# Kernel optimization log

Hardware: AMD Instinct MI355X
Metric: run time of the kernel (lower is better)

## Reference

```python
import jax, jax.numpy as jnp
import numpy as np

B, S, E, FFN, Q = 8, 2048, 512, 2048, 8


def setup_inputs() -> dict:
    key = jax.random.key(0)
    k0, k1, k2, k3 = jax.random.split(key, 4)
    x = jax.random.normal(k0, (B, S, E), dtype=jnp.float32)
    ry = jax.random.normal(k1, (Q,), dtype=jnp.float32)  # trainable RY angles
    w1 = jax.random.normal(k2, (FFN, Q), dtype=jnp.float32) / np.sqrt(Q).astype(np.float32)
    b1 = jnp.zeros((FFN,), dtype=jnp.float32)
    w2 = jax.random.normal(k3, (E, FFN), dtype=jnp.float32) / np.sqrt(FFN).astype(np.float32)
    b2 = jnp.zeros((E,), dtype=jnp.float32)
    return {"x": x, "ry": ry, "w1": w1, "b1": b1, "w2": w2, "b2": b2}


def reference(x, ry, w1, b1, w2, b2):
    # Quantum layer: each qubit i starts in |0>, gets RX(x[..., i]) then RY(ry[i]),
    # then PauliZ expectation. Product state => closed form <Z_i> = cos(x_i) * cos(ry_i).
    nq = ry.shape[0]
    z = jnp.cos(x[..., :nq]) * jnp.cos(ry)  # [B, S, Q]
    # dropout is identity in eval mode
    h = jnp.einsum("bsq,fq->bsf", z, w1) + b1  # fc1
    return jnp.einsum("bsf,ef->bse", jax.nn.relu(h), w2) + b2  # fc2
```

## Files before the change

### kernel.cpp

```cpp
#include <hip/hip_runtime.h>
#include <cstdint>
#include <cstddef>


typedef __attribute__((ext_vector_type(8))) short s16x8;
typedef __attribute__((ext_vector_type(4))) float f32x4;

__device__ __forceinline__ unsigned short f2bf(float f) {
  unsigned int u = __float_as_uint(f);
  unsigned int r = u + 0x7fffu + ((u >> 16) & 1u);
  return (unsigned short)(r >> 16);
}

__device__ __forceinline__ void async_copy16(const void* g, void* l) {
  __builtin_amdgcn_global_load_lds(
      (const __attribute__((address_space(1))) void*)(uintptr_t)g,
      (__attribute__((address_space(3))) void*)(unsigned int)(uintptr_t)l,
      16, 0, 0);
}

__global__ __launch_bounds__(256) void k_w2(const float* __restrict__ w2,
                                            unsigned short* __restrict__ img) {
  const int n = blockIdx.x;
  const int t = threadIdx.x;
  const int s = t >> 2, quad = t & 3;
  const float* src = w2 + (size_t)n * 2048 + t * 8;
  float4 a = *(const float4*)src;
  float4 b = *(const float4*)(src + 4);
  uint4 pk;
  pk.x = f2bf(a.x) | ((unsigned)f2bf(a.y) << 16);
  pk.y = f2bf(a.z) | ((unsigned)f2bf(a.w) << 16);
  pk.z = f2bf(b.x) | ((unsigned)f2bf(b.y) << 16);
  pk.w = f2bf(b.z) | ((unsigned)f2bf(b.w) << 16);
  const int nt = n >> 8, nl = n & 255, nhi = nl >> 4, nlo = nl & 15;
  const size_t ci = (size_t)(nt * 64 + s) * 1024 + nhi * 64 + quad * 16 + nlo;
  *(uint4*)(img + ci * 8) = pk;
}

__global__ __launch_bounds__(256, 2) void k_fused(
    const float* __restrict__ x, const float* __restrict__ ry,
    const float* __restrict__ w1, const float* __restrict__ b1,
    const unsigned short* __restrict__ w2b, const float* __restrict__ b2,
    float* __restrict__ C) {
  __shared__ unsigned short As[2][64 * 32];
  __shared__ unsigned short Bs[3][256 * 32];
  __shared__ float b1s[2048];

  const int t = threadIdx.x;
  const int lane = t & 63;
  const int w = t >> 6;
  const int mt = (int)(blockIdx.x >> 1);
  const int nt = (int)(blockIdx.x & 1);
  const int r0 = mt * 64;
  const int c0 = nt * 256;
  const int fp = t & 15;
  const int rq = t >> 4;

  float zr[4][8];
  {
    float4 ra = *(const float4*)ry;
    float4 rb = *(const float4*)(ry + 4);
    float cy[8] = {__cosf(ra.x), __cosf(ra.y), __cosf(ra.z), __cosf(ra.w),
                   __cosf(rb.x), __cosf(rb.y), __cosf(rb.z), __cosf(rb.w)};
#pragma unroll
    for (int r = 0; r < 4; ++r) {
      const float* xr = x + (size_t)(r0 + rq * 4 + r) * 512;
      float4 x0 = *(const float4*)xr;
      float4 x1 = *(const float4*)(xr + 4);
      zr[r][0] = __cosf(x0.x) * cy[0];
      zr[r][1] = __cosf(x0.y) * cy[1];
      zr[r][2] = __cosf(x0.z) * cy[2];
      zr[r][3] = __cosf(x0.w) * cy[3];
      zr[r][4] = __cosf(x1.x) * cy[4];
      zr[r][5] = __cosf(x1.y) * cy[5];
      zr[r][6] = __cosf(x1.z) * cy[6];
      zr[r][7] = __cosf(x1.w) * cy[7];
    }
  }
  __builtin_amdgcn_sched_barrier(0);

  const unsigned short* gB = w2b + (size_t)nt * 524288 + t * 8;
  char* lB = (char*)Bs + t * 16;
  auto stage = [&](int s, int buf) {
#pragma unroll
    for (int p = 0; p < 4; ++p)
      async_copy16(gB + (size_t)s * 8192 + p * 2048,
                   lB + buf * 16384 + p * 4096);
  };
  async_copy16(b1 + (size_t)t * 4, (char*)b1s + (size_t)t * 16);
  async_copy16(b1 + (size_t)(t + 256) * 4, (char*)b1s + (size_t)(t + 256) * 16);
  stage(0, 0);
  stage(1, 1);
  __builtin_amdgcn_sched_barrier(0);

  f32x4 wA0, wA1, wA2, wA3, wB0, wB1, wB2, wB3;
  {
    const f32x4* p0 = (const f32x4*)(w1 + fp * 16);
    wA0 = p0[0]; wA1 = p0[1]; wA2 = p0[2]; wA3 = p0[3];
    const f32x4* p1 = (const f32x4*)(w1 + 256 + fp * 16);
    wB0 = p1[0]; wB1 = p1[1]; wB2 = p1[2]; wB3 = p1[3];
  }

  asm volatile("s_waitcnt vmcnt(12) lgkmcnt(0)" ::: "memory");
  __builtin_amdgcn_sched_barrier(0);
  __builtin_amdgcn_s_barrier();

  const int q0 = rq & 1;
  const int koct = fp >> 2, fpl = fp & 3;
  const int sA_off = ((koct ^ ((rq * 2) & 3)) << 4) + fpl * 4;
  const int sB_off = ((koct ^ ((rq * 2 + 1) & 3)) << 4) + fpl * 4;
  const int rw0 = ((rq * 4 + 0) ^ q0) * 64;
  const int rw1 = ((rq * 4 + 1) ^ q0) * 64;
  const int rw2 = ((rq * 4 + 2) ^ q0) * 64;
  const int rw3 = ((rq * 4 + 3) ^ q0) * 64;

  auto act = [&](int s, int buf, const f32x4& v0, const f32x4& v1,
                 const f32x4& v2, const f32x4& v3) {
    const float bb0 = b1s[s * 32 + fp * 2];
    const float bb1 = b1s[s * 32 + fp * 2 + 1];
    unsigned int u0, u1, u2, u3;
#define ACT_ROW(R, UD)                                                      \
  {                                                                         \
    float h0 = bb0, h1 = bb1;                                               \
    h0 += zr[R][0] * v0[0]; h1 += zr[R][0] * v2[0];                         \
    h0 += zr[R][1] * v0[1]; h1 += zr[R][1] * v2[1];                         \
    h0 += zr[R][2] * v0[2]; h1 += zr[R][2] * v2[2];                         \
    h0 += zr[R][3] * v0[3]; h1 += zr[R][3] * v2[3];                         \
    h0 += zr[R][4] * v1[0]; h1 += zr[R][4] * v3[0];                         \
    h0 += zr[R][5] * v1[1]; h1 += zr[R][5] * v3[1];                         \
    h0 += zr[R][6] * v1[2]; h1 += zr[R][6] * v3[2];                         \
    h0 += zr[R][7] * v1[3]; h1 += zr[R][7] * v3[3];                         \
    h0 = fmaxf(h0, 0.0f);                                                   \
    h1 = fmaxf(h1, 0.0f);                                                   \
    asm("v_cvt_pk_bf16_f32 %0, %1, %2" : "=v"(UD) : "v"(h0), "v"(h1));      \
  }
    ACT_ROW(0, u0) ACT_ROW(1, u1) ACT_ROW(2, u2) ACT_ROW(3, u3)
#undef ACT_ROW
    char* base = (char*)As + buf * 4096;
    *(unsigned int*)(base + rw0 + sA_off) = q0 ? u1 : u0;
    *(unsigned int*)(base + rw1 + sA_off) = q0 ? u0 : u1;
    *(unsigned int*)(base + rw2 + sB_off) = q0 ? u3 : u2;
    *(unsigned int*)(base + rw3 + sB_off) = q0 ? u2 : u3;
  };

  act(0, 0, wA0, wA1, wA2, wA3);

  const int wn = w * 64;
  const int fr = lane & 15;
  const int quad = lane >> 4;
  const char* pAb =
      (const char*)As + fr * 64 + ((quad ^ ((fr >> 1) & 3)) << 4);
  const char* pBb = (const char*)Bs + w * 4096 + quad * 256 + fr * 16;

  f32x4 acc[4][4];
#pragma unroll
  for (int i = 0; i < 4; ++i)
#pragma unroll
    for (int j = 0; j < 4; ++j) acc[i][j] = (f32x4){0.f, 0.f, 0.f, 0.f};

#define BODY(KT, BUF, BUF2, L0, L1, L2, L3, U0, U1, U2, U3, PRE, ACTG, VMC) \
  {                                                                         \
    asm volatile("s_waitcnt vmcnt(" VMC ") lgkmcnt(0)" ::: "memory");       \
    __builtin_amdgcn_sched_barrier(0);                                      \
    __builtin_amdgcn_s_barrier();                                           \
    if (PRE) {                                                              \
      stage((KT) + 2, BUF2);                                                \
      const f32x4* wp =                                                     \
          (const f32x4*)(w1 + (size_t)((KT) + 2) * 256 + fp * 16);          \
      L0 = wp[0]; L1 = wp[1]; L2 = wp[2]; L3 = wp[3];                       \
    }                                                                       \
    s16x8 af[4], bfv[4];                                                    \
    {                                                                       \
      const char* pA = pAb + ((KT) & 1) * 4096;                             \
      const char* pB = pBb + (BUF) * 16384;                                 \
      af[0] = *(const s16x8*)(pA);                                          \
      af[1] = *(const s16x8*)(pA + 1024);                                   \
      af[2] = *(const s16x8*)(pA + 2048);                                   \
      af[3] = *(const s16x8*)(pA + 3072);                                   \
      bfv[0] = *(const s16x8*)(pB);                                         \
      bfv[1] = *(const s16x8*)(pB + 1024);                                  \
      bfv[2] = *(const s16x8*)(pB + 2048);                                  \
      bfv[3] = *(const s16x8*)(pB + 3072);                                  \
    }                                                                       \
    if (ACTG) act((KT) + 1, ((KT) + 1) & 1, U0, U1, U2, U3);                \
    __builtin_amdgcn_s_setprio(1);                                          \
    _Pragma("unroll") for (int i = 0; i < 4; ++i)                           \
        _Pragma("unroll") for (int j = 0; j < 4; ++j) acc[i][j] =           \
        __builtin_amdgcn_mfma_f32_16x16x32_bf16(af[i], bfv[j], acc[i][j],   \
                                                0, 0, 0);                   \
    __builtin_amdgcn_s_setprio(0);                                          \
  }

  for (int kt = 0; kt < 60; kt += 6) {
    BODY(kt + 0, 0, 2, wA0, wA1, wA2, wA3, wB0, wB1, wB2, wB3, true, true, "8");
    BODY(kt + 1, 1, 0, wB0, wB1, wB2, wB3, wA0, wA1, wA2, wA3, true, true, "8");
    BODY(kt + 2, 2, 1, wA0, wA1, wA2, wA3, wB0, wB1, wB2, wB3, true, true, "8");
    BODY(kt + 3, 0, 2, wB0, wB1, wB2, wB3, wA0, wA1, wA2, wA3, true, true, "8");
    BODY(kt + 4, 1, 0, wA0, wA1, wA2, wA3, wB0, wB1, wB2, wB3, true, true, "8");
    BODY(kt + 5, 2, 1, wB0, wB1, wB2, wB3, wA0, wA1, wA2, wA3, true, true, "8");
  }
  BODY(60, 0, 2, wA0, wA1, wA2, wA3, wB0, wB1, wB2, wB3, true, true, "8");
  BODY(61, 1, 0, wB0, wB1, wB2, wB3, wA0, wA1, wA2, wA3, true, true, "8");
  BODY(62, 2, 1, wA0, wA1, wA2, wA3, wB0, wB1, wB2, wB3, false, true, "8");
  BODY(63, 0, 2, wB0, wB1, wB2, wB3, wA0, wA1, wA2, wA3, false, false, "4");
#undef BODY

  float bias[4];
#pragma unroll
  for (int j = 0; j < 4; ++j) bias[j] = b2[c0 + wn + j * 16 + fr];
#pragma unroll
  for (int i = 0; i < 4; ++i) {
    const int rbase = r0 + i * 16 + quad * 4;
#pragma unroll
    for (int rr = 0; rr < 4; ++rr) {
      float* crow = C + (size_t)(rbase + rr) * 512;
#pragma unroll
      for (int j = 0; j < 4; ++j)
        crow[c0 + wn + j * 16 + fr] = acc[i][j][rr] + bias[j];
    }
  }
}

__global__ __launch_bounds__(256) void k_naive(
    const float* __restrict__ x, const float* __restrict__ ry,
    const float* __restrict__ w1, const float* __restrict__ b1,
    const float* __restrict__ w2, const float* __restrict__ b2,
    float* __restrict__ out) {
  __shared__ float zsh[8];
  __shared__ float acts[2048];
  const int r = blockIdx.x;
  const int t = threadIdx.x;
  if (t < 8) zsh[t] = __cosf(x[(size_t)r * 512 + t]) * __cosf(ry[t]);
  __syncthreads();
  float z[8];
#pragma unroll
  for (int q = 0; q < 8; ++q) z[q] = zsh[q];
#pragma unroll
  for (int i = 0; i < 8; ++i) {
    const int f = t * 8 + i;
    const float* wr = w1 + (size_t)f * 8;
    float4 a = *(const float4*)wr;
    float4 b = *(const float4*)(wr + 4);
    float h = b1[f] + z[0] * a.x + z[1] * a.y + z[2] * a.z + z[3] * a.w +
              z[4] * b.x + z[5] * b.y + z[6] * b.z + z[7] * b.w;
    acts[f] = fmaxf(h, 0.0f);
  }
  __syncthreads();
  for (int ee = 0; ee < 2; ++ee) {
    const int e = t + ee * 256;
    const float* wr = w2 + (size_t)e * 2048;
    float acc = b2[e];
    for (int f = 0; f < 2048; f += 4) {
      float4 wv = *(const float4*)(wr + f);
      float4 av = *(const float4*)(acts + f);
      acc += av.x * wv.x + av.y * wv.y + av.z * wv.z + av.w * wv.w;
    }
    out[(size_t)r * 512 + e] = acc;
  }
}

extern "C" void kernel_launch(void* const* d_in, const int* in_sizes, int n_in,
                              void* d_out, int out_size, void* d_ws,
                              size_t ws_size, hipStream_t stream) {
  const float* x  = (const float*)d_in[0];
  const float* ry = (const float*)d_in[1];
  const float* w1 = (const float*)d_in[2];
  const float* b1 = (const float*)d_in[3];
  const float* w2 = (const float*)d_in[4];
  const float* b2 = (const float*)d_in[5];
  float* out = (float*)d_out;

  const size_t w2b_bytes = (size_t)512 * 2048 * 2;
  if (ws_size < w2b_bytes) {
    k_naive<<<dim3(16384), dim3(256), 0, stream>>>(x, ry, w1, b1, w2, b2, out);
    return;
  }
  unsigned short* w2b = (unsigned short*)d_ws;
  k_w2<<<dim3(512), dim3(256), 0, stream>>>(w2, w2b);
  k_fused<<<dim3(512), dim3(256), 0, stream>>>(x, ry, w1, b1, w2b, b2, out);
}
```

Measured before the change: 150.7 us.

## Double block to 512 threads, splitting M across two warp groups

Raises the fused kernel to 512 threads per block, with 8 waves arranged 2 (M) by 4 (N). Each thread now computes two activation rows instead of four and holds half the accumulators, and each thread issues half as many async copies per stage. The waitcnt thresholds and the LDS swizzle for A are reworked to match. The aim is more waves per CU to hide latency and lower per-thread register pressure, at the cost of more barrier participants and a __launch_bounds__(512,4) occupancy target that may force register spills.

```diff
diff --git a/kernel.cpp b/kernel.cpp
--- a/kernel.cpp
+++ b/kernel.cpp
@@ -37,7 +37,7 @@
   *(uint4*)(img + ci * 8) = pk;
 }
 
-__global__ __launch_bounds__(256, 2) void k_fused(
+__global__ __launch_bounds__(512, 4) void k_fused(
     const float* __restrict__ x, const float* __restrict__ ry,
     const float* __restrict__ w1, const float* __restrict__ b1,
     const unsigned short* __restrict__ w2b, const float* __restrict__ b2,
@@ -54,17 +54,17 @@
   const int r0 = mt * 64;
   const int c0 = nt * 256;
   const int fp = t & 15;
-  const int rq = t >> 4;
-
-  float zr[4][8];
+  const int rw = t >> 4;
+
+  float zr[2][8];
   {
     float4 ra = *(const float4*)ry;
     float4 rb = *(const float4*)(ry + 4);
     float cy[8] = {__cosf(ra.x), __cosf(ra.y), __cosf(ra.z), __cosf(ra.w),
                    __cosf(rb.x), __cosf(rb.y), __cosf(rb.z), __cosf(rb.w)};
 #pragma unroll
-    for (int r = 0; r < 4; ++r) {
-      const float* xr = x + (size_t)(r0 + rq * 4 + r) * 512;
+    for (int r = 0; r < 2; ++r) {
+      const float* xr = x + (size_t)(r0 + rw * 2 + r) * 512;
       float4 x0 = *(const float4*)xr;
       float4 x1 = *(const float4*)(xr + 4);
       zr[r][0] = __cosf(x0.x) * cy[0];
@@ -82,43 +82,35 @@
   const unsigned short* gB = w2b + (size_t)nt * 524288 + t * 8;
   char* lB = (char*)Bs + t * 16;
   auto stage = [&](int s, int buf) {
-#pragma unroll
-    for (int p = 0; p < 4; ++p)
-      async_copy16(gB + (size_t)s * 8192 + p * 2048,
-                   lB + buf * 16384 + p * 4096);
+    async_copy16(gB + (size_t)s * 8192, lB + buf * 16384);
+    async_copy16(gB + (size_t)s * 8192 + 4096, lB + buf * 16384 + 8192);
   };
   async_copy16(b1 + (size_t)t * 4, (char*)b1s + (size_t)t * 16);
-  async_copy16(b1 + (size_t)(t + 256) * 4, (char*)b1s + (size_t)(t + 256) * 16);
   stage(0, 0);
-  stage(1, 1);
-  __builtin_amdgcn_sched_barrier(0);
-
   f32x4 wA0, wA1, wA2, wA3, wB0, wB1, wB2, wB3;
   {
     const f32x4* p0 = (const f32x4*)(w1 + fp * 16);
     wA0 = p0[0]; wA1 = p0[1]; wA2 = p0[2]; wA3 = p0[3];
+  }
+  stage(1, 1);
+  {
     const f32x4* p1 = (const f32x4*)(w1 + 256 + fp * 16);
     wB0 = p1[0]; wB1 = p1[1]; wB2 = p1[2]; wB3 = p1[3];
   }
 
-  asm volatile("s_waitcnt vmcnt(12) lgkmcnt(0)" ::: "memory");
+  asm volatile("s_waitcnt vmcnt(6) lgkmcnt(0)" ::: "memory");
   __builtin_amdgcn_sched_barrier(0);
   __builtin_amdgcn_s_barrier();
 
-  const int q0 = rq & 1;
   const int koct = fp >> 2, fpl = fp & 3;
-  const int sA_off = ((koct ^ ((rq * 2) & 3)) << 4) + fpl * 4;
-  const int sB_off = ((koct ^ ((rq * 2 + 1) & 3)) << 4) + fpl * 4;
-  const int rw0 = ((rq * 4 + 0) ^ q0) * 64;
-  const int rw1 = ((rq * 4 + 1) ^ q0) * 64;
-  const int rw2 = ((rq * 4 + 2) ^ q0) * 64;
-  const int rw3 = ((rq * 4 + 3) ^ q0) * 64;
+  const int s_off = ((koct ^ (rw & 3)) << 4) + fpl * 4;
+  char* aswr = (char*)As + rw * 128 + s_off;
 
   auto act = [&](int s, int buf, const f32x4& v0, const f32x4& v1,
                  const f32x4& v2, const f32x4& v3) {
     const float bb0 = b1s[s * 32 + fp * 2];
     const float bb1 = b1s[s * 32 + fp * 2 + 1];
-    unsigned int u0, u1, u2, u3;
+    unsigned int u0, u1;
 #define ACT_ROW(R, UD)                                                      \
   {                                                                         \
     float h0 = bb0, h1 = bb1;                                               \
@@ -134,27 +126,26 @@
     h1 = fmaxf(h1, 0.0f);                                                   \
     asm("v_cvt_pk_bf16_f32 %0, %1, %2" : "=v"(UD) : "v"(h0), "v"(h1));      \
   }
-    ACT_ROW(0, u0) ACT_ROW(1, u1) ACT_ROW(2, u2) ACT_ROW(3, u3)
+    ACT_ROW(0, u0) ACT_ROW(1, u1)
 #undef ACT_ROW
-    char* base = (char*)As + buf * 4096;
-    *(unsigned int*)(base + rw0 + sA_off) = q0 ? u1 : u0;
-    *(unsigned int*)(base + rw1 + sA_off) = q0 ? u0 : u1;
-    *(unsigned int*)(base + rw2 + sB_off) = q0 ? u3 : u2;
-    *(unsigned int*)(base + rw3 + sB_off) = q0 ? u2 : u3;
+    char* dst = aswr + buf * 4096;
+    *(unsigned int*)(dst) = u0;
+    *(unsigned int*)(dst + 64) = u1;
   };
 
   act(0, 0, wA0, wA1, wA2, wA3);
 
-  const int wn = w * 64;
+  const int wm = (w >> 2) * 32;
+  const int wn = (w & 3) * 64;
   const int fr = lane & 15;
   const int quad = lane >> 4;
-  const char* pAb =
-      (const char*)As + fr * 64 + ((quad ^ ((fr >> 1) & 3)) << 4);
-  const char* pBb = (const char*)Bs + w * 4096 + quad * 256 + fr * 16;
-
-  f32x4 acc[4][4];
-#pragma unroll
-  for (int i = 0; i < 4; ++i)
+  const char* pAb = (const char*)As + wm * 64 + fr * 64 +
+                    ((quad ^ ((fr >> 1) & 3)) << 4);
+  const char* pBb = (const char*)Bs + (w & 3) * 4096 + quad * 256 + fr * 16;
+
+  f32x4 acc[2][4];
+#pragma unroll
+  for (int i = 0; i < 2; ++i)
 #pragma unroll
     for (int j = 0; j < 4; ++j) acc[i][j] = (f32x4){0.f, 0.f, 0.f, 0.f};
 
@@ -169,14 +160,12 @@
           (const f32x4*)(w1 + (size_t)((KT) + 2) * 256 + fp * 16);          \
       L0 = wp[0]; L1 = wp[1]; L2 = wp[2]; L3 = wp[3];                       \
     }                                                                       \
-    s16x8 af[4], bfv[4];                                                    \
+    s16x8 af[2], bfv[4];                                                    \
     {                                                                       \
       const char* pA = pAb + ((KT) & 1) * 4096;                             \
       const char* pB = pBb + (BUF) * 16384;                                 \
       af[0] = *(const s16x8*)(pA);                                          \
       af[1] = *(const s16x8*)(pA + 1024);                                   \
-      af[2] = *(const s16x8*)(pA + 2048);                                   \
-      af[3] = *(const s16x8*)(pA + 3072);                                   \
       bfv[0] = *(const s16x8*)(pB);                                         \
       bfv[1] = *(const s16x8*)(pB + 1024);                                  \
       bfv[2] = *(const s16x8*)(pB + 2048);                                  \
@@ -184,7 +173,7 @@
     }                                                                       \
     if (ACTG) act((KT) + 1, ((KT) + 1) & 1, U0, U1, U2, U3);                \
     __builtin_amdgcn_s_setprio(1);                                          \
-    _Pragma("unroll") for (int i = 0; i < 4; ++i)                           \
+    _Pragma("unroll") for (int i = 0; i < 2; ++i)                           \
         _Pragma("unroll") for (int j = 0; j < 4; ++j) acc[i][j] =           \
         __builtin_amdgcn_mfma_f32_16x16x32_bf16(af[i], bfv[j], acc[i][j],   \
                                                 0, 0, 0);                   \
@@ -192,25 +181,25 @@
   }
 
   for (int kt = 0; kt < 60; kt += 6) {
-    BODY(kt + 0, 0, 2, wA0, wA1, wA2, wA3, wB0, wB1, wB2, wB3, true, true, "8");
-    BODY(kt + 1, 1, 0, wB0, wB1, wB2, wB3, wA0, wA1, wA2, wA3, true, true, "8");
-    BODY(kt + 2, 2, 1, wA0, wA1, wA2, wA3, wB0, wB1, wB2, wB3, true, true, "8");
-    BODY(kt + 3, 0, 2, wB0, wB1, wB2, wB3, wA0, wA1, wA2, wA3, true, true, "8");
-    BODY(kt + 4, 1, 0, wA0, wA1, wA2, wA3, wB0, wB1, wB2, wB3, true, true, "8");
-    BODY(kt + 5, 2, 1, wB0, wB1, wB2, wB3, wA0, wA1, wA2, wA3, true, true, "8");
-  }
-  BODY(60, 0, 2, wA0, wA1, wA2, wA3, wB0, wB1, wB2, wB3, true, true, "8");
-  BODY(61, 1, 0, wB0, wB1, wB2, wB3, wA0, wA1, wA2, wA3, true, true, "8");
-  BODY(62, 2, 1, wA0, wA1, wA2, wA3, wB0, wB1, wB2, wB3, false, true, "8");
-  BODY(63, 0, 2, wB0, wB1, wB2, wB3, wA0, wA1, wA2, wA3, false, false, "4");
+    BODY(kt + 0, 0, 2, wA0, wA1, wA2, wA3, wB0, wB1, wB2, wB3, true, true, "6");
+    BODY(kt + 1, 1, 0, wB0, wB1, wB2, wB3, wA0, wA1, wA2, wA3, true, true, "6");
+    BODY(kt + 2, 2, 1, wA0, wA1, wA2, wA3, wB0, wB1, wB2, wB3, true, true, "6");
+    BODY(kt + 3, 0, 2, wB0, wB1, wB2, wB3, wA0, wA1, wA2, wA3, true, true, "6");
+    BODY(kt + 4, 1, 0, wA0, wA1, wA2, wA3, wB0, wB1, wB2, wB3, true, true, "6");
+    BODY(kt + 5, 2, 1, wB0, wB1, wB2, wB3, wA0, wA1, wA2, wA3, true, true, "6");
+  }
+  BODY(60, 0, 2, wA0, wA1, wA2, wA3, wB0, wB1, wB2, wB3, true, true, "6");
+  BODY(61, 1, 0, wB0, wB1, wB2, wB3, wA0, wA1, wA2, wA3, true, true, "6");
+  BODY(62, 2, 1, wA0, wA1, wA2, wA3, wB0, wB1, wB2, wB3, false, true, "6");
+  BODY(63, 0, 2, wB0, wB1, wB2, wB3, wA0, wA1, wA2, wA3, false, false, "0");
 #undef BODY
 
   float bias[4];
 #pragma unroll
   for (int j = 0; j < 4; ++j) bias[j] = b2[c0 + wn + j * 16 + fr];
 #pragma unroll
-  for (int i = 0; i < 4; ++i) {
-    const int rbase = r0 + i * 16 + quad * 4;
+  for (int i = 0; i < 2; ++i) {
+    const int rbase = r0 + wm + i * 16 + quad * 4;
 #pragma unroll
     for (int rr = 0; rr < 4; ++rr) {
       float* crow = C + (size_t)(rbase + rr) * 512;
@@ -277,5 +266,5 @@
   }
   unsigned short* w2b = (unsigned short*)d_ws;
   k_w2<<<dim3(512), dim3(256), 0, stream>>>(w2, w2b);
-  k_fused<<<dim3(512), dim3(256), 0, stream>>>(x, ry, w1, b1, w2b, b2, out);
-}
+  k_fused<<<dim3(512), dim3(512), 0, stream>>>(x, ry, w1, b1, w2b, b2, out);
+}
```

After: 177.8 us. +18.0%, slower.

## Load W2 fragments directly from global into registers instead of LDS staging

Applied to the files above, without the earlier changes.

Drops the triple-buffered LDS staging of the pre-packed bf16 W2 tiles. Each wave now loads its MFMA B fragments straight from global memory into registers, double-buffered one k-step ahead. The barrier schedule changes to match: wait on vmcnt before the MFMAs and put a single barrier at the end of each step. This removes LDS traffic and frees LDS for occupancy, at the cost of exposing global-load latency with only one step of prefetch and using more registers.

```diff
diff --git a/kernel.cpp b/kernel.cpp
--- a/kernel.cpp
+++ b/kernel.cpp
@@ -43,7 +43,6 @@
     const unsigned short* __restrict__ w2b, const float* __restrict__ b2,
     float* __restrict__ C) {
   __shared__ unsigned short As[2][64 * 32];
-  __shared__ unsigned short Bs[3][256 * 32];
   __shared__ float b1s[2048];
 
   const int t = threadIdx.x;
@@ -55,6 +54,8 @@
   const int c0 = nt * 256;
   const int fp = t & 15;
   const int rq = t >> 4;
+  const int fr = lane & 15;
+  const int quad = lane >> 4;
 
   float zr[4][8];
   {
@@ -79,20 +80,22 @@
   }
   __builtin_amdgcn_sched_barrier(0);
 
-  const unsigned short* gB = w2b + (size_t)nt * 524288 + t * 8;
-  char* lB = (char*)Bs + t * 16;
-  auto stage = [&](int s, int buf) {
-#pragma unroll
-    for (int p = 0; p < 4; ++p)
-      async_copy16(gB + (size_t)s * 8192 + p * 2048,
-                   lB + buf * 16384 + p * 4096);
-  };
+  const char* gBb =
+      (const char*)w2b +
+      ((size_t)nt * 64 * 1024 + (size_t)w * 256 + quad * 16 + fr) * 16;
+#define LOADB(S, D)                                        \
+  {                                                        \
+    const char* p_ = gBb + (size_t)(S) * 16384;            \
+    D[0] = *(const s16x8*)(p_);                            \
+    D[1] = *(const s16x8*)(p_ + 1024);                     \
+    D[2] = *(const s16x8*)(p_ + 2048);                     \
+    D[3] = *(const s16x8*)(p_ + 3072);                     \
+  }
+
   async_copy16(b1 + (size_t)t * 4, (char*)b1s + (size_t)t * 16);
   async_copy16(b1 + (size_t)(t + 256) * 4, (char*)b1s + (size_t)(t + 256) * 16);
-  stage(0, 0);
-  stage(1, 1);
-  __builtin_amdgcn_sched_barrier(0);
-
+  s16x8 Bp[4], Bq[4];
+  LOADB(0, Bp);
   f32x4 wA0, wA1, wA2, wA3, wB0, wB1, wB2, wB3;
   {
     const f32x4* p0 = (const f32x4*)(w1 + fp * 16);
@@ -100,8 +103,7 @@
     const f32x4* p1 = (const f32x4*)(w1 + 256 + fp * 16);
     wB0 = p1[0]; wB1 = p1[1]; wB2 = p1[2]; wB3 = p1[3];
   }
-
-  asm volatile("s_waitcnt vmcnt(12) lgkmcnt(0)" ::: "memory");
+  asm volatile("s_waitcnt vmcnt(0) lgkmcnt(0)" ::: "memory");
   __builtin_amdgcn_sched_barrier(0);
   __builtin_amdgcn_s_barrier();
 
@@ -144,13 +146,13 @@
   };
 
   act(0, 0, wA0, wA1, wA2, wA3);
+  asm volatile("s_waitcnt lgkmcnt(0)" ::: "memory");
+  __builtin_amdgcn_sched_barrier(0);
+  __builtin_amdgcn_s_barrier();
 
   const int wn = w * 64;
-  const int fr = lane & 15;
-  const int quad = lane >> 4;
   const char* pAb =
       (const char*)As + fr * 64 + ((quad ^ ((fr >> 1) & 3)) << 4);
-  const char* pBb = (const char*)Bs + w * 4096 + quad * 256 + fr * 16;
 
   f32x4 acc[4][4];
 #pragma unroll
@@ -158,52 +160,49 @@
 #pragma unroll
     for (int j = 0; j < 4; ++j) acc[i][j] = (f32x4){0.f, 0.f, 0.f, 0.f};
 
-#define BODY(KT, BUF, BUF2, L0, L1, L2, L3, U0, U1, U2, U3, PRE, ACTG, VMC) \
+#define BODY(KT, BU, BL, WU0, WU1, WU2, WU3, WL0, WL1, WL2, WL3, BPRE,      \
+             WPRE, ACTG, VMC)                                               \
   {                                                                         \
-    asm volatile("s_waitcnt vmcnt(" VMC ") lgkmcnt(0)" ::: "memory");       \
-    __builtin_amdgcn_sched_barrier(0);                                      \
-    __builtin_amdgcn_s_barrier();                                           \
-    if (PRE) {                                                              \
-      stage((KT) + 2, BUF2);                                                \
+    if (BPRE) LOADB((KT) + 1, BL);                                          \
+    if (WPRE) {                                                             \
       const f32x4* wp =                                                     \
           (const f32x4*)(w1 + (size_t)((KT) + 2) * 256 + fp * 16);          \
-      L0 = wp[0]; L1 = wp[1]; L2 = wp[2]; L3 = wp[3];                       \
+      WL0 = wp[0]; WL1 = wp[1]; WL2 = wp[2]; WL3 = wp[3];                   \
     }                                                                       \
-    s16x8 af[4], bfv[4];                                                    \
+    asm volatile("s_waitcnt vmcnt(" VMC ")" ::: "memory");                  \
+    __builtin_amdgcn_sched_barrier(0);                                      \
+    s16x8 af[4];                                                            \
     {                                                                       \
       const char* pA = pAb + ((KT) & 1) * 4096;                             \
-      const char* pB = pBb + (BUF) * 16384;                                 \
       af[0] = *(const s16x8*)(pA);                                          \
       af[1] = *(const s16x8*)(pA + 1024);                                   \
       af[2] = *(const s16x8*)(pA + 2048);                                   \
       af[3] = *(const s16x8*)(pA + 3072);                                   \
-      bfv[0] = *(const s16x8*)(pB);                                         \
-      bfv[1] = *(const s16x8*)(pB + 1024);                                  \
-      bfv[2] = *(const s16x8*)(pB + 2048);                                  \
-      bfv[3] = *(const s16x8*)(pB + 3072);                                  \
     }                                                                       \
-    if (ACTG) act((KT) + 1, ((KT) + 1) & 1, U0, U1, U2, U3);                \
+    if (ACTG) act((KT) + 1, ((KT) + 1) & 1, WU0, WU1, WU2, WU3);            \
+    asm volatile("s_waitcnt lgkmcnt(0)" ::: "memory");                      \
+    __builtin_amdgcn_sched_barrier(0);                                      \
     __builtin_amdgcn_s_setprio(1);                                          \
     _Pragma("unroll") for (int i = 0; i < 4; ++i)                           \
         _Pragma("unroll") for (int j = 0; j < 4; ++j) acc[i][j] =           \
-        __builtin_amdgcn_mfma_f32_16x16x32_bf16(af[i], bfv[j], acc[i][j],   \
+        __builtin_amdgcn_mfma_f32_16x16x32_bf16(af[i], BU[j], acc[i][j],    \
                                                 0, 0, 0);                   \
     __builtin_amdgcn_s_setprio(0);                                          \
-  }
-
-  for (int kt = 0; kt < 60; kt += 6) {
-    BODY(kt + 0, 0, 2, wA0, wA1, wA2, wA3, wB0, wB1, wB2, wB3, true, true, "8");
-    BODY(kt + 1, 1, 0, wB0, wB1, wB2, wB3, wA0, wA1, wA2, wA3, true, true, "8");
-    BODY(kt + 2, 2, 1, wA0, wA1, wA2, wA3, wB0, wB1, wB2, wB3, true, true, "8");
-    BODY(kt + 3, 0, 2, wB0, wB1, wB2, wB3, wA0, wA1, wA2, wA3, true, true, "8");
-    BODY(kt + 4, 1, 0, wA0, wA1, wA2, wA3, wB0, wB1, wB2, wB3, true, true, "8");
-    BODY(kt + 5, 2, 1, wB0, wB1, wB2, wB3, wA0, wA1, wA2, wA3, true, true, "8");
-  }
-  BODY(60, 0, 2, wA0, wA1, wA2, wA3, wB0, wB1, wB2, wB3, true, true, "8");
-  BODY(61, 1, 0, wB0, wB1, wB2, wB3, wA0, wA1, wA2, wA3, true, true, "8");
-  BODY(62, 2, 1, wA0, wA1, wA2, wA3, wB0, wB1, wB2, wB3, false, true, "8");
-  BODY(63, 0, 2, wB0, wB1, wB2, wB3, wA0, wA1, wA2, wA3, false, false, "4");
+    __builtin_amdgcn_s_barrier();                                           \
+  }
+
+  for (int kt = 0; kt < 62; kt += 2) {
+    BODY(kt, Bp, Bq, wB0, wB1, wB2, wB3, wA0, wA1, wA2, wA3, true, true,
+         true, "8");
+    BODY(kt + 1, Bq, Bp, wA0, wA1, wA2, wA3, wB0, wB1, wB2, wB3, true, true,
+         true, "8");
+  }
+  BODY(62, Bp, Bq, wB0, wB1, wB2, wB3, wA0, wA1, wA2, wA3, true, false, true,
+       "4");
+  BODY(63, Bq, Bp, wA0, wA1, wA2, wA3, wB0, wB1, wB2, wB3, false, false,
+       false, "0");
 #undef BODY
+#undef LOADB
 
   float bias[4];
 #pragma unroll
```

After: 138.8 us. -7.9%, faster.
